# Performance work log

Measured on AMD Instinct MI355X. Metric: run time of the kernel, lower is better.

The kernel has to match this reference:

```python
import jax, jax.numpy as jnp
import numpy as np

TAU = 1.0
EPS = 1e-8  # F.cosine_similarity eps


def _cl(X, Y):
    # Pairwise cosine similarity via L2-normalize + single GEMM (N,D)@(D,N)
    Xn = X / jnp.maximum(jnp.linalg.norm(X, axis=1, keepdims=True), EPS)
    Yn = Y / jnp.maximum(jnp.linalg.norm(Y, axis=1, keepdims=True), EPS)
    sim = Xn @ Yn.T  # [N, N], sim[i, j] = cos(X_i, Y_j)
    e = jnp.exp(sim / TAU)
    pos = jnp.diagonal(e)               # exp(diag(sim)/tau), [N]
    neg = jnp.sum(e, axis=0) - pos      # column sums minus positive, [N]
    return -jnp.log(pos / neg).reshape(X.shape[0], 1)


def setup_inputs() -> dict:
    key = jax.random.key(0)
    ks = jax.random.split(key, 6)
    N, D1, D2, DO = 8192, 1024, 768, 256
    X = jax.random.normal(ks[0], (N, D1), dtype=jnp.float32)
    Y = jax.random.normal(ks[1], (N, D2), dtype=jnp.float32)
    # nn.Linear params (kaiming-uniform-ish scale)
    Wx = jax.random.uniform(ks[2], (DO, D1), jnp.float32, -1, 1) / np.sqrt(D1)
    bx = jax.random.uniform(ks[3], (DO,), jnp.float32, -1, 1) / np.sqrt(D1)
    Wy = jax.random.uniform(ks[4], (DO, D2), jnp.float32, -1, 1) / np.sqrt(D2)
    by = jax.random.uniform(ks[5], (DO,), jnp.float32, -1, 1) / np.sqrt(D2)
    return {"X": X, "Y": Y, "Wx": Wx, "bx": bx, "Wy": Wy, "by": by}


def reference(X, Y, Wx, bx, Wy, by):
    Xp = X @ Wx.T + bx  # proj_x
    Yp = Y @ Wy.T + by  # proj_y
    return _cl(Xp, Yp) + _cl(Yp, Xp)  # [N, 1]
```

## Files before the change

kernel.cpp:

```cpp
#include <hip/hip_runtime.h>
#include <hip/hip_bf16.h>

typedef __bf16 bf16_t;
typedef __bf16 bf16x8 __attribute__((ext_vector_type(8)));
typedef float  f32x4  __attribute__((ext_vector_type(4)));
typedef int    i32x8  __attribute__((ext_vector_type(8)));

__device__ __forceinline__ bf16x8 pack8(f32x4 a, f32x4 b) {
    bf16x8 h = { (bf16_t)a.x, (bf16_t)a.y, (bf16_t)a.z, (bf16_t)a.w,
                 (bf16_t)b.x, (bf16_t)b.y, (bf16_t)b.z, (bf16_t)b.w };
    return h;
}

__device__ __forceinline__ void gl_lds16(const void* g, void* l) {
    __builtin_amdgcn_global_load_lds(
        (const __attribute__((address_space(1))) unsigned int*)g,
        (__attribute__((address_space(3))) unsigned int*)l, 16, 0, 0);
}

#if __has_builtin(__builtin_amdgcn_cvt_pk_fp8_f32)
__device__ __forceinline__ unsigned char cvt1_e4m3(float x) {
    return (unsigned char)(__builtin_amdgcn_cvt_pk_fp8_f32(x, x, 0, false) & 0xff);
}
#else
__device__ __forceinline__ unsigned char cvt1_e4m3(float x) {
    unsigned u = __float_as_uint(x);
    unsigned sign = (u >> 24) & 0x80u;
    float a = fabsf(x);
    if (a < 7.8125e-3f) { int q = (int)(a * 512.0f + 0.5f); return (unsigned char)(sign | q); }
    if (a >= 448.0f) return (unsigned char)(sign | 0x7E);
    unsigned au = u & 0x7FFFFFFFu;
    unsigned lsb = (au >> 20) & 1u;
    au += 0x7FFFFu + lsb;
    int exp = (int)(au >> 23) - 127;
    unsigned man = (au >> 20) & 7u;
    return (unsigned char)(sign | ((unsigned)(exp + 7) << 3) | man);
}
#endif

__device__ __forceinline__ int frag_off_k(int row16, int k) {
    return ((k >> 6) << 10) + (((k >> 3) & 3) << 8) + (row16 << 4)
         + (((k >> 5) & 1) << 3) + (k & 7);
}

__global__ __launch_bounds__(256) void wconv(
    const float* __restrict__ Wx, const float* __restrict__ Wy,
    bf16_t* __restrict__ Wxt, bf16_t* __restrict__ Wyt,
    float* __restrict__ sums)
{
    int id = blockIdx.x * 256 + threadIdx.x;
    if (blockIdx.x < 64) sums[id] = 0.0f;

    int row, k0, K;
    const float* W;
    bf16_t* Wt;
    if (id < 32768) { W = Wx; Wt = Wxt; K = 1024; row = id >> 7; k0 = (id & 127) << 3; }
    else { int c = id - 32768; W = Wy; Wt = Wyt; K = 768; row = c / 96; k0 = (c % 96) << 3; }

    f32x4 lo = *reinterpret_cast<const f32x4*>(&W[(size_t)row * K + k0]);
    f32x4 hi = *reinterpret_cast<const f32x4*>(&W[(size_t)row * K + k0 + 4]);
    size_t off = (size_t)(row >> 4) * 16 * K + frag_off_k(row & 15, k0);
    *reinterpret_cast<bf16x8*>(Wt + off) = pack8(lo, hi);
}

__global__ __launch_bounds__(512, 2) void proj_norm(
    const float* __restrict__ X, const float* __restrict__ Y,
    const bf16_t* __restrict__ Wxt, const float* __restrict__ bxp,
    const bf16_t* __restrict__ Wyt, const float* __restrict__ byp,
    unsigned char* __restrict__ Xt, unsigned char* __restrict__ Yt)
{
    __shared__ float Abuf[2][64 * 64];
    __shared__ unsigned char obuf[16384];
    __shared__ float ssqL[4][64];

    const int tid  = threadIdx.x;
    const int lane = tid & 63;
    const int wave = tid >> 6;
    const int quad = lane >> 4;
    const int c16  = lane & 15;
    const int rg   = wave >> 2;
    const int cg   = wave & 3;

    const bool isY = blockIdx.x >= 128;
    const float*  A    = isY ? Y   : X;
    const bf16_t* Wt   = isY ? Wyt : Wxt;
    const float*  bias = isY ? byp : bxp;
    unsigned char* dst = isY ? Yt  : Xt;
    const int K = isY ? 768 : 1024;
    const int S = K >> 6;
    const int rowBase = (blockIdx.x & 127) * 64;

    auto stage = [&](int s, int b) {
        #pragma unroll
        for (int t = 0; t < 2; ++t) {
            int r0  = (wave * 2 + t) * 4;
            int row = r0 + (lane >> 4);
            int gch = (lane & 15) ^ (row & 15);
            gl_lds16(&A[(size_t)(rowBase + row) * K + s * 64 + gch * 4],
                     &Abuf[b][r0 * 64]);
        }
    };

    auto aFrag = [&](int b, int mf, int s2) -> bf16x8 {
        int row = rg * 32 + mf * 16 + c16;
        int e   = s2 * 8 + quad * 2;
        const float* base = &Abuf[b][row * 64];
        f32x4 lo = *reinterpret_cast<const f32x4*>(base + ((e ^ c16) << 2));
        f32x4 hi = *reinterpret_cast<const f32x4*>(base + (((e + 1) ^ c16) << 2));
        return pack8(lo, hi);
    };

    const bf16_t* pB[4];
    #pragma unroll
    for (int nf = 0; nf < 4; ++nf)
        pB[nf] = Wt + (size_t)(cg * 4 + nf) * 16 * K + quad * 256 + c16 * 16;

    f32x4 acc[2][4] = {};
    stage(0, 0);

    for (int s = 0; s < S; ++s) {
        const int b = s & 1;
        __syncthreads();
        if (s + 1 < S) stage(s + 1, b ^ 1);
        #pragma unroll
        for (int s2 = 0; s2 < 2; ++s2) {
            bf16x8 bF[4];
            #pragma unroll
            for (int nf = 0; nf < 4; ++nf)
                bF[nf] = *reinterpret_cast<const bf16x8*>(pB[nf] + s * 1024 + s2 * 8);
            #pragma unroll
            for (int mf = 0; mf < 2; ++mf) {
                bf16x8 aF = aFrag(b, mf, s2);
                #pragma unroll
                for (int nf = 0; nf < 4; ++nf)
                    acc[mf][nf] = __builtin_amdgcn_mfma_f32_16x16x32_bf16(
                        aF, bF[nf], acc[mf][nf], 0, 0, 0);
            }
        }
    }

    #pragma unroll
    for (int nf = 0; nf < 4; ++nf) {
        float bb = bias[cg * 64 + nf * 16 + c16];
        #pragma unroll
        for (int mf = 0; mf < 2; ++mf)
            #pragma unroll
            for (int r = 0; r < 4; ++r) acc[mf][nf][r] += bb;
    }

    #pragma unroll
    for (int mf = 0; mf < 2; ++mf)
        #pragma unroll
        for (int r = 0; r < 4; ++r) {
            float v = 0.f;
            #pragma unroll
            for (int nf = 0; nf < 4; ++nf) v += acc[mf][nf][r] * acc[mf][nf][r];
            v += __shfl_xor(v, 1, 64);
            v += __shfl_xor(v, 2, 64);
            v += __shfl_xor(v, 4, 64);
            v += __shfl_xor(v, 8, 64);
            if (c16 == 0) ssqL[cg][rg * 32 + mf * 16 + quad * 4 + r] = v;
        }
    __syncthreads();

    #pragma unroll
    for (int mf = 0; mf < 2; ++mf)
        #pragma unroll
        for (int r = 0; r < 4; ++r) {
            int lr = rg * 32 + mf * 16 + quad * 4 + r;
            float t = ssqL[0][lr] + ssqL[1][lr] + ssqL[2][lr] + ssqL[3][lr];
            float inv = 1.0f / fmaxf(sqrtf(t), 1e-8f);
            #pragma unroll
            for (int nf = 0; nf < 4; ++nf) {
                int k = cg * 64 + nf * 16 + c16;
                obuf[((lr >> 4) << 12) + ((k >> 5) << 9) + ((lr & 15) << 5) + (k & 31)] =
                    cvt1_e4m3(acc[mf][nf][r] * inv);
            }
        }
    __syncthreads();

    const f32x4* src = reinterpret_cast<const f32x4*>(&obuf[tid * 32]);
    f32x4* g = reinterpret_cast<f32x4*>(dst + (size_t)rowBase * 256 + tid * 32);
    g[0] = src[0];
    g[1] = src[1];
}

__global__ __launch_bounds__(256) void sim_gemm(
    const unsigned char* __restrict__ Xt, const unsigned char* __restrict__ Yt,
    float* __restrict__ rowsum, float* __restrict__ colsum,
    float* __restrict__ pos)
{
    __shared__ float red[256];

    const int tid  = threadIdx.x;
    const int lane = tid & 63;
    const int wave = tid >> 6;
    const int quad = lane >> 4;
    const int c16  = lane & 15;
    const int wy   = wave >> 1;
    const int wx   = wave & 1;

    const int id = blockIdx.x;
    const int b2 = id >> 3;
    const int colBlk = (id & 7) * 8 + (b2 >> 6);
    const int rowBlk = b2 & 63;
    const int rowBase = rowBlk * 128;
    const int colBase = colBlk * 128;

    const i32x8* pa[4];
    const i32x8* pb[4];
    #pragma unroll
    for (int mf = 0; mf < 4; ++mf)
        pa[mf] = reinterpret_cast<const i32x8*>(
            Xt + (size_t)(rowBase + wy * 64 + mf * 16) * 256 + quad * 512 + c16 * 32);
    #pragma unroll
    for (int nf = 0; nf < 4; ++nf)
        pb[nf] = reinterpret_cast<const i32x8*>(
            Yt + (size_t)(colBase + wx * 64 + nf * 16) * 256 + quad * 512 + c16 * 32);

    f32x4 acc[4][4] = {};

    i32x8 A0[4], B0[4], A1[4], B1[4];
    #pragma unroll
    for (int i = 0; i < 4; ++i) { A0[i] = pa[i][0];  B0[i] = pb[i][0]; }
    #pragma unroll
    for (int i = 0; i < 4; ++i) { A1[i] = pa[i][64]; B1[i] = pb[i][64]; }

    #pragma unroll
    for (int mf = 0; mf < 4; ++mf)
        #pragma unroll
        for (int nf = 0; nf < 4; ++nf)
            acc[mf][nf] = __builtin_amdgcn_mfma_scale_f32_16x16x128_f8f6f4(
                A0[mf], B0[nf], acc[mf][nf], 0, 0, 0, 127, 0, 127);
    #pragma unroll
    for (int mf = 0; mf < 4; ++mf)
        #pragma unroll
        for (int nf = 0; nf < 4; ++nf)
            acc[mf][nf] = __builtin_amdgcn_mfma_scale_f32_16x16x128_f8f6f4(
                A1[mf], B1[nf], acc[mf][nf], 0, 0, 0, 127, 0, 127);

    #pragma unroll
    for (int mf = 0; mf < 4; ++mf)
        #pragma unroll
        for (int nf = 0; nf < 4; ++nf)
            #pragma unroll
            for (int r = 0; r < 4; ++r)
                acc[mf][nf][r] = __expf(acc[mf][nf][r]);

    if (rowBase == colBase) {
        #pragma unroll
        for (int mf = 0; mf < 4; ++mf)
            #pragma unroll
            for (int nf = 0; nf < 4; ++nf)
                #pragma unroll
                for (int r = 0; r < 4; ++r) {
                    int lrow = wy * 64 + mf * 16 + quad * 4 + r;
                    int lcol = wx * 64 + nf * 16 + c16;
                    if (lrow == lcol) pos[rowBase + lrow] = acc[mf][nf][r];
                }
    }

    float rs[4][4];
    #pragma unroll
    for (int mf = 0; mf < 4; ++mf)
        #pragma unroll
        for (int r = 0; r < 4; ++r) {
            float v = acc[mf][0][r] + acc[mf][1][r] + acc[mf][2][r] + acc[mf][3][r];
            v += __shfl_xor(v, 1, 64);
            v += __shfl_xor(v, 2, 64);
            v += __shfl_xor(v, 4, 64);
            v += __shfl_xor(v, 8, 64);
            rs[mf][r] = v;
        }

    float cs[4];
    #pragma unroll
    for (int nf = 0; nf < 4; ++nf) {
        float v = 0.f;
        #pragma unroll
        for (int mf = 0; mf < 4; ++mf)
            #pragma unroll
            for (int r = 0; r < 4; ++r)
                v += acc[mf][nf][r];
        v += __shfl_xor(v, 16, 64);
        v += __shfl_xor(v, 32, 64);
        cs[nf] = v;
    }

    red[tid] = 0.f;
    __syncthreads();

    if (c16 == 0) {
        #pragma unroll
        for (int mf = 0; mf < 4; ++mf)
            #pragma unroll
            for (int r = 0; r < 4; ++r)
                atomicAdd(&red[wy * 64 + mf * 16 + quad * 4 + r], rs[mf][r]);
    }
    if (quad == 0) {
        #pragma unroll
        for (int nf = 0; nf < 4; ++nf)
            atomicAdd(&red[128 + wx * 64 + nf * 16 + c16], cs[nf]);
    }
    __syncthreads();

    if (tid < 128) atomicAdd(&rowsum[rowBase + tid], red[tid]);
    else           atomicAdd(&colsum[colBase + tid - 128], red[tid]);
}

__global__ __launch_bounds__(256) void finalize(
    const float* __restrict__ rowsum, const float* __restrict__ colsum,
    const float* __restrict__ pos, float* __restrict__ out)
{
    int i = blockIdx.x * 256 + threadIdx.x;
    float p = pos[i];
    out[i] = logf(colsum[i] - p) + logf(rowsum[i] - p) - 2.0f * logf(p);
}

extern "C" void kernel_launch(void* const* d_in, const int* in_sizes, int n_in,
                              void* d_out, int out_size, void* d_ws, size_t ws_size,
                              hipStream_t stream) {
    const float* X  = (const float*)d_in[0];
    const float* Y  = (const float*)d_in[1];
    const float* Wx = (const float*)d_in[2];
    const float* bx = (const float*)d_in[3];
    const float* Wy = (const float*)d_in[4];
    const float* by = (const float*)d_in[5];
    float* out = (float*)d_out;

    char* ws = (char*)d_ws;
    unsigned char* Xt  = (unsigned char*)(ws);
    unsigned char* Yt  = (unsigned char*)(ws + (2u << 20));
    bf16_t*        Wxt = (bf16_t*)(ws + (4u << 20));
    bf16_t*        Wyt = (bf16_t*)(ws + (4u << 20) + (512u << 10));
    float* rowsum = (float*)(ws + (5u << 20));
    float* colsum = rowsum + 8192;
    float* pos    = colsum + 8192;

    wconv<<<224, 256, 0, stream>>>(Wx, Wy, Wxt, Wyt, rowsum);
    proj_norm<<<256, 512, 0, stream>>>(X, Y, Wxt, bx, Wyt, by, Xt, Yt);
    sim_gemm<<<4096, 256, 0, stream>>>(Xt, Yt, rowsum, colsum, pos);
    finalize<<<32, 256, 0, stream>>>(rowsum, colsum, pos, out);
}
```

Baseline: 160.2 us.

## Process four row tiles per block in sim_gemm, reusing B fragments in registers

Each sim_gemm block now covers a 512x128 strip instead of a 128x128 tile, so the grid shrinks from 4096 to 1024 blocks. The Y fragments stay in registers across four row tiles, and the next A tile is prefetched after the MFMAs are issued. Column sums accumulate in registers and are flushed once per block, which cuts global atomics, and the shared-memory atomics become plain stores into a two-slot buffer. The cost is more serialized work per block, extra barriers inside the loop, and higher register pressure under launch_bounds(256,2).

```diff
diff --git a/kernel.cpp b/kernel.cpp
--- a/kernel.cpp
+++ b/kernel.cpp
@@ -185,12 +185,12 @@
     g[1] = src[1];
 }
 
-__global__ __launch_bounds__(256) void sim_gemm(
+__global__ __launch_bounds__(256, 2) void sim_gemm(
     const unsigned char* __restrict__ Xt, const unsigned char* __restrict__ Yt,
     float* __restrict__ rowsum, float* __restrict__ colsum,
     float* __restrict__ pos)
 {
-    __shared__ float red[256];
+    __shared__ float red2[2][128];
 
     const int tid  = threadIdx.x;
     const int lane = tid & 63;
@@ -202,110 +202,135 @@
 
     const int id = blockIdx.x;
     const int b2 = id >> 3;
-    const int colBlk = (id & 7) * 8 + (b2 >> 6);
-    const int rowBlk = b2 & 63;
-    const int rowBase = rowBlk * 128;
+    const int colBlk = (id & 7) * 8 + (b2 >> 4);
+    const int rowGrp = b2 & 15;
     const int colBase = colBlk * 128;
 
-    const i32x8* pa[4];
-    const i32x8* pb[4];
-    #pragma unroll
-    for (int mf = 0; mf < 4; ++mf)
-        pa[mf] = reinterpret_cast<const i32x8*>(
+    i32x8 B0[4], B1[4];
+    #pragma unroll
+    for (int nf = 0; nf < 4; ++nf) {
+        const i32x8* p = reinterpret_cast<const i32x8*>(
+            Yt + (size_t)(colBase + wx * 64 + nf * 16) * 256 + quad * 512 + c16 * 32);
+        B0[nf] = p[0];
+        B1[nf] = p[64];
+    }
+
+    auto aPtr = [&](int rowBase, int mf) {
+        return reinterpret_cast<const i32x8*>(
             Xt + (size_t)(rowBase + wy * 64 + mf * 16) * 256 + quad * 512 + c16 * 32);
-    #pragma unroll
-    for (int nf = 0; nf < 4; ++nf)
-        pb[nf] = reinterpret_cast<const i32x8*>(
-            Yt + (size_t)(colBase + wx * 64 + nf * 16) * 256 + quad * 512 + c16 * 32);
-
-    f32x4 acc[4][4] = {};
-
-    i32x8 A0[4], B0[4], A1[4], B1[4];
-    #pragma unroll
-    for (int i = 0; i < 4; ++i) { A0[i] = pa[i][0];  B0[i] = pb[i][0]; }
-    #pragma unroll
-    for (int i = 0; i < 4; ++i) { A1[i] = pa[i][64]; B1[i] = pb[i][64]; }
-
-    #pragma unroll
-    for (int mf = 0; mf < 4; ++mf)
-        #pragma unroll
-        for (int nf = 0; nf < 4; ++nf)
-            acc[mf][nf] = __builtin_amdgcn_mfma_scale_f32_16x16x128_f8f6f4(
-                A0[mf], B0[nf], acc[mf][nf], 0, 0, 0, 127, 0, 127);
-    #pragma unroll
-    for (int mf = 0; mf < 4; ++mf)
-        #pragma unroll
-        for (int nf = 0; nf < 4; ++nf)
-            acc[mf][nf] = __builtin_amdgcn_mfma_scale_f32_16x16x128_f8f6f4(
-                A1[mf], B1[nf], acc[mf][nf], 0, 0, 0, 127, 0, 127);
-
-    #pragma unroll
-    for (int mf = 0; mf < 4; ++mf)
-        #pragma unroll
-        for (int nf = 0; nf < 4; ++nf)
-            #pragma unroll
-            for (int r = 0; r < 4; ++r)
-                acc[mf][nf][r] = __expf(acc[mf][nf][r]);
-
-    if (rowBase == colBase) {
+    };
+
+    i32x8 A0[4], A1[4];
+    #pragma unroll
+    for (int mf = 0; mf < 4; ++mf) {
+        const i32x8* p = aPtr(rowGrp * 512, mf);
+        A0[mf] = p[0];
+        A1[mf] = p[64];
+    }
+
+    float cs[4] = {0.f, 0.f, 0.f, 0.f};
+
+    for (int t = 0; t < 4; ++t) {
+        const int rowBase = rowGrp * 512 + t * 128;
+
+        f32x4 acc[4][4] = {};
         #pragma unroll
         for (int mf = 0; mf < 4; ++mf)
             #pragma unroll
             for (int nf = 0; nf < 4; ++nf)
-                #pragma unroll
-                for (int r = 0; r < 4; ++r) {
-                    int lrow = wy * 64 + mf * 16 + quad * 4 + r;
-                    int lcol = wx * 64 + nf * 16 + c16;
-                    if (lrow == lcol) pos[rowBase + lrow] = acc[mf][nf][r];
-                }
-    }
-
-    float rs[4][4];
-    #pragma unroll
-    for (int mf = 0; mf < 4; ++mf)
-        #pragma unroll
-        for (int r = 0; r < 4; ++r) {
-            float v = acc[mf][0][r] + acc[mf][1][r] + acc[mf][2][r] + acc[mf][3][r];
-            v += __shfl_xor(v, 1, 64);
-            v += __shfl_xor(v, 2, 64);
-            v += __shfl_xor(v, 4, 64);
-            v += __shfl_xor(v, 8, 64);
-            rs[mf][r] = v;
-        }
-
-    float cs[4];
+                acc[mf][nf] = __builtin_amdgcn_mfma_scale_f32_16x16x128_f8f6f4(
+                    A0[mf], B0[nf], acc[mf][nf], 0, 0, 0, 127, 0, 127);
+        #pragma unroll
+        for (int mf = 0; mf < 4; ++mf)
+            #pragma unroll
+            for (int nf = 0; nf < 4; ++nf)
+                acc[mf][nf] = __builtin_amdgcn_mfma_scale_f32_16x16x128_f8f6f4(
+                    A1[mf], B1[nf], acc[mf][nf], 0, 0, 0, 127, 0, 127);
+
+        if (t < 3) {
+            #pragma unroll
+            for (int mf = 0; mf < 4; ++mf) {
+                const i32x8* p = aPtr(rowBase + 128, mf);
+                A0[mf] = p[0];
+                A1[mf] = p[64];
+            }
+        }
+
+        #pragma unroll
+        for (int mf = 0; mf < 4; ++mf)
+            #pragma unroll
+            for (int nf = 0; nf < 4; ++nf)
+                #pragma unroll
+                for (int r = 0; r < 4; ++r)
+                    acc[mf][nf][r] = __expf(acc[mf][nf][r]);
+
+        if (rowBase == colBase) {
+            #pragma unroll
+            for (int mf = 0; mf < 4; ++mf)
+                #pragma unroll
+                for (int nf = 0; nf < 4; ++nf)
+                    #pragma unroll
+                    for (int r = 0; r < 4; ++r) {
+                        int lrow = wy * 64 + mf * 16 + quad * 4 + r;
+                        int lcol = wx * 64 + nf * 16 + c16;
+                        if (lrow == lcol) pos[rowBase + lrow] = acc[mf][nf][r];
+                    }
+        }
+
+        float rs[4][4];
+        #pragma unroll
+        for (int mf = 0; mf < 4; ++mf)
+            #pragma unroll
+            for (int r = 0; r < 4; ++r) {
+                float v = acc[mf][0][r] + acc[mf][1][r] + acc[mf][2][r] + acc[mf][3][r];
+                v += __shfl_xor(v, 1, 64);
+                v += __shfl_xor(v, 2, 64);
+                v += __shfl_xor(v, 4, 64);
+                v += __shfl_xor(v, 8, 64);
+                rs[mf][r] = v;
+            }
+
+        #pragma unroll
+        for (int nf = 0; nf < 4; ++nf) {
+            float v = 0.f;
+            #pragma unroll
+            for (int mf = 0; mf < 4; ++mf)
+                #pragma unroll
+                for (int r = 0; r < 4; ++r)
+                    v += acc[mf][nf][r];
+            cs[nf] += v;
+        }
+
+        __syncthreads();
+        if (c16 == 0) {
+            #pragma unroll
+            for (int mf = 0; mf < 4; ++mf)
+                #pragma unroll
+                for (int r = 0; r < 4; ++r)
+                    red2[wx][wy * 64 + mf * 16 + quad * 4 + r] = rs[mf][r];
+        }
+        __syncthreads();
+        if (tid < 128)
+            atomicAdd(&rowsum[rowBase + tid], red2[0][tid] + red2[1][tid]);
+    }
+
+    float csr[4];
     #pragma unroll
     for (int nf = 0; nf < 4; ++nf) {
-        float v = 0.f;
-        #pragma unroll
-        for (int mf = 0; mf < 4; ++mf)
-            #pragma unroll
-            for (int r = 0; r < 4; ++r)
-                v += acc[mf][nf][r];
+        float v = cs[nf];
         v += __shfl_xor(v, 16, 64);
         v += __shfl_xor(v, 32, 64);
-        cs[nf] = v;
-    }
-
-    red[tid] = 0.f;
+        csr[nf] = v;
+    }
     __syncthreads();
-
-    if (c16 == 0) {
-        #pragma unroll
-        for (int mf = 0; mf < 4; ++mf)
-            #pragma unroll
-            for (int r = 0; r < 4; ++r)
-                atomicAdd(&red[wy * 64 + mf * 16 + quad * 4 + r], rs[mf][r]);
-    }
     if (quad == 0) {
         #pragma unroll
         for (int nf = 0; nf < 4; ++nf)
-            atomicAdd(&red[128 + wx * 64 + nf * 16 + c16], cs[nf]);
+            red2[wy][wx * 64 + nf * 16 + c16] = csr[nf];
     }
     __syncthreads();
-
-    if (tid < 128) atomicAdd(&rowsum[rowBase + tid], red[tid]);
-    else           atomicAdd(&colsum[colBase + tid - 128], red[tid]);
+    if (tid < 128)
+        atomicAdd(&colsum[colBase + tid], red2[0][tid] + red2[1][tid]);
 }
 
 __global__ __launch_bounds__(256) void finalize(
@@ -339,6 +364,6 @@
 
     wconv<<<224, 256, 0, stream>>>(Wx, Wy, Wxt, Wyt, rowsum);
     proj_norm<<<256, 512, 0, stream>>>(X, Y, Wxt, bx, Wyt, by, Xt, Yt);
-    sim_gemm<<<4096, 256, 0, stream>>>(Xt, Yt, rowsum, colsum, pos);
+    sim_gemm<<<1024, 256, 0, stream>>>(Xt, Yt, rowsum, colsum, pos);
     finalize<<<32, 256, 0, stream>>>(rowsum, colsum, pos, out);
 }
```

New measurement: 155.8 us. 2.8% less time.
